# Optimization experiments

Measured on AMD Instinct MI355X. Metric: run time of the kernel, lower is better.

Reference implementation:

```python
import jax, jax.numpy as jnp
import numpy as np

D_MODEL = 1024
N_HEADS = 16
D_HEAD = D_MODEL // N_HEADS
EPS_LN = 1e-5
EPS_GATE = 1e-5
EPS_DEN = 1e-5


def setup_inputs() -> dict:
    key = jax.random.key(0)
    ks = jax.random.split(key, 4)
    B, T, D = 1, 2048, D_MODEL
    x = jax.random.normal(ks[0], (B, T, D), dtype=jnp.float32)
    # Linear weights scaled like torch default init (~1/sqrt(fan_in))
    s = 1.0 / np.sqrt(D)
    qkv_w = jax.random.normal(ks[1], (3 * D, D), dtype=jnp.float32) * s
    gate_w = jax.random.normal(ks[2], (D, D), dtype=jnp.float32) * s
    proj_w = jax.random.normal(ks[3], (D, D), dtype=jnp.float32) * s
    return {
        "x": x,
        "ln_g": jnp.ones((D,), jnp.float32),
        "ln_b": jnp.zeros((D,), jnp.float32),
        "qkv_w": qkv_w,
        "qkv_b": jnp.zeros((3 * D,), jnp.float32),
        "gate_w": gate_w,
        "gate_b": jnp.zeros((D,), jnp.float32),
        "proj_w": proj_w,
        "proj_b": jnp.zeros((D,), jnp.float32),
    }


def _linear(x, w, b):
    # torch nn.Linear: y = x @ W^T + b, W is (out, in)
    return jnp.einsum("btd,od->bto", x, w) + b


def reference(x, ln_g, ln_b, qkv_w, qkv_b, gate_w, gate_b, proj_w, proj_b):
    B, T, D = x.shape
    H, Dh = N_HEADS, D_HEAD

    # LayerNorm
    mu = jnp.mean(x, axis=-1, keepdims=True)
    var = jnp.mean((x - mu) ** 2, axis=-1, keepdims=True)
    x_norm = (x - mu) / jnp.sqrt(var + EPS_LN) * ln_g + ln_b

    qkv = _linear(x_norm, qkv_w, qkv_b)
    q, k, v = jnp.split(qkv, 3, axis=-1)

    # concept gate on raw x
    gate_sig = jax.nn.sigmoid(_linear(x, gate_w, gate_b))
    gate_norm = gate_sig / (jnp.mean(gate_sig, axis=-1, keepdims=True) + EPS_GATE)
    q = q * gate_norm
    k = k * gate_norm

    # (B,T,D) -> (B,H,T,Dh)
    def heads(t):
        return t.reshape(B, T, H, Dh).transpose(0, 2, 1, 3)

    q, k, v = heads(q).astype(jnp.float32), heads(k).astype(jnp.float32), heads(v).astype(jnp.float32)

    q = jax.nn.elu(q) + 1.0
    k = jax.nn.elu(k) + 1.0

    # causal linear attention via cumsum of outer products (same math as source)
    kv = jnp.einsum("bhtd,bhtm->bhtdm", k, v)        # (B,H,T,Dh,Dh)
    kv_cum = jnp.cumsum(kv, axis=2)
    out_num = jnp.einsum("bhtd,bhtdm->bhtm", q, kv_cum)
    k_cum = jnp.cumsum(k, axis=2)
    out_den = jnp.einsum("bhtd,bhtd->bht", q, k_cum)[..., None] + EPS_DEN
    out = out_num / out_den                           # (B,H,T,Dh)

    out = out.astype(x_norm.dtype).transpose(0, 2, 1, 3).reshape(B, T, D)
    return _linear(out, proj_w, proj_b)
```

## Files before the change

kernel.cpp:

```cpp
#include <hip/hip_runtime.h>
#include <hip/hip_bf16.h>
#include <math.h>

#define T_SEQ 2048
#define DM 1024
#define NH 16
#define DH 64
#define CHUNK 64
#define NCHUNK (T_SEQ / CHUNK)

typedef __hip_bfloat16 bf16;
typedef __attribute__((ext_vector_type(8))) short short8;
typedef __attribute__((ext_vector_type(4))) short short4v;
typedef __attribute__((ext_vector_type(4))) float f32x4;

static __device__ __forceinline__ short f2b_bits(float f) {
  bf16 t = __float2bfloat16(f);
  short s;
  __builtin_memcpy(&s, &t, 2);
  return s;
}
static __device__ __forceinline__ float b2f(short s) {
  unsigned int u = ((unsigned int)(unsigned short)s) << 16;
  float f;
  __builtin_memcpy(&f, &u, 4);
  return f;
}

static __device__ __forceinline__ float gelu1(float raw, float gate, float inv) {
  float x = raw * gate * inv;
  return x > 0.f ? x + 1.f : __expf(x);
}

static __device__ __forceinline__ void gload16(const void* g, void* l) {
  __builtin_amdgcn_global_load_lds((const __attribute__((address_space(1))) void*)g,
                                   (__attribute__((address_space(3))) void*)l, 16, 0, 0);
}

#define PREP_WBLOCKS (5 * DM * DM / 4 / 256)
__global__ __launch_bounds__(256) void prep_kernel(
    const float* __restrict__ x, const float* __restrict__ g,
    const float* __restrict__ b, const float* __restrict__ qkv_w,
    const float* __restrict__ gate_w, const float* __restrict__ proj_w,
    bf16* __restrict__ xn, bf16* __restrict__ xbf,
    bf16* __restrict__ wqkv, bf16* __restrict__ wgate, bf16* __restrict__ wproj,
    float* __restrict__ gate_accum) {
  const int blk = blockIdx.x;
  if (blk < T_SEQ) {
    const int row = blk;
    if (row < 8) gate_accum[row * 256 + threadIdx.x] = 0.f;
    const float* xr = x + (size_t)row * DM;
    float vals[4];
    float s = 0.f, s2 = 0.f;
#pragma unroll
    for (int i = 0; i < 4; i++) {
      float v = xr[threadIdx.x + i * 256];
      vals[i] = v;
      s += v;
      s2 += v * v;
    }
#pragma unroll
    for (int m = 1; m < 64; m <<= 1) {
      s += __shfl_xor(s, m, 64);
      s2 += __shfl_xor(s2, m, 64);
    }
    __shared__ float red[8];
    const int wid = threadIdx.x >> 6;
    if ((threadIdx.x & 63) == 0) {
      red[wid] = s;
      red[4 + wid] = s2;
    }
    __syncthreads();
    s = red[0] + red[1] + red[2] + red[3];
    s2 = red[4] + red[5] + red[6] + red[7];
    const float mean = s * (1.f / DM);
    const float var = s2 * (1.f / DM) - mean * mean;
    const float rstd = rsqrtf(var + 1e-5f);
#pragma unroll
    for (int i = 0; i < 4; i++) {
      int idx = threadIdx.x + i * 256;
      float v = (vals[i] - mean) * rstd * g[idx] + b[idx];
      xn[(size_t)row * DM + idx] = __float2bfloat16(v);
      xbf[(size_t)row * DM + idx] = __float2bfloat16(vals[i]);
    }
  } else {
    constexpr int NQ = 3 * DM * DM / 4, NS = DM * DM / 4;
    int i = (blk - T_SEQ) * 256 + threadIdx.x;
    const float* src;
    bf16* dst;
    int j;
    if (i < NQ) { src = qkv_w; dst = wqkv; j = i; }
    else if (i < NQ + NS) { src = gate_w; dst = wgate; j = i - NQ; }
    else { src = proj_w; dst = wproj; j = i - NQ - NS; }
    float4 v = ((const float4*)src)[j];
    short4v sv;
    sv.x = f2b_bits(v.x); sv.y = f2b_bits(v.y); sv.z = f2b_bits(v.z); sv.w = f2b_bits(v.w);
    *(short4v*)&dst[j * 4] = sv;
  }
}

__global__ __launch_bounds__(256) void gemm_gateqkv(
    const bf16* __restrict__ xbf, const bf16* __restrict__ xn,
    const bf16* __restrict__ wg, const bf16* __restrict__ wq,
    const float* __restrict__ gate_b, const float* __restrict__ qkv_b,
    short* __restrict__ Gb, float* __restrict__ gate_accum,
    short* __restrict__ Qb, short* __restrict__ Kb, short* __restrict__ Vb) {
  constexpr int K = 1024;
  __shared__ __align__(16) short As[2 * 128 * 32];
  __shared__ __align__(16) short Bs[2 * 128 * 32];

  const int tid = threadIdx.x;
  const int wid = tid >> 6, lane = tid & 63;
  const int wm = wid >> 1, wn = wid & 1;
  const int lm = lane & 15, quad = lane >> 4;

  const bool isGate = blockIdx.y < 8;
  const int m0 = blockIdx.x * 128;
  const int n0 = isGate ? blockIdx.y * 128 : (blockIdx.y - 8) * 128;
  const short* Ag = (const short*)(isGate ? xbf : xn);
  const short* Wg = (const short*)(isGate ? wg : wq);

  f32x4 zero = {0.f, 0.f, 0.f, 0.f};
  f32x4 acc[4][4];
#pragma unroll
  for (int i = 0; i < 4; i++)
#pragma unroll
    for (int j = 0; j < 4; j++) acc[i][j] = zero;

  for (int kb = 0; kb < K; kb += 64) {
    __syncthreads();
#pragma unroll
    for (int sec = 0; sec < 2; sec++) {
#pragma unroll
      for (int it = 0; it < 2; it++) {
        const int idx = it * 256 + tid;
        const int row = idx >> 2, seg = (idx & 3) * 8;
        gload16(&Ag[(size_t)(m0 + row) * K + kb + sec * 32 + seg],
                &As[sec * 4096 + (it * 256 + wid * 64) * 8]);
        gload16(&Wg[(size_t)(n0 + row) * K + kb + sec * 32 + seg],
                &Bs[sec * 4096 + (it * 256 + wid * 64) * 8]);
      }
    }
    __syncthreads();
#pragma unroll
    for (int sec = 0; sec < 2; sec++) {
      short8 afr[4], bfr[4];
#pragma unroll
      for (int i = 0; i < 4; i++) {
        afr[i] = *(const short8*)&As[sec * 4096 + (wm * 64 + i * 16 + lm) * 32 + quad * 8];
        bfr[i] = *(const short8*)&Bs[sec * 4096 + (wn * 64 + i * 16 + lm) * 32 + quad * 8];
      }
#pragma unroll
      for (int i = 0; i < 4; i++)
#pragma unroll
        for (int j = 0; j < 4; j++)
          acc[i][j] = __builtin_amdgcn_mfma_f32_16x16x32_bf16(afr[i], bfr[j], acc[i][j], 0, 0, 0);
    }
  }

  if (isGate) {
    float* red = (float*)As;
    __syncthreads();
#pragma unroll
    for (int i = 0; i < 4; i++) {
#pragma unroll
      for (int r = 0; r < 4; r++) {
        const int rowl = wm * 64 + i * 16 + quad * 4 + r;
        const int row = m0 + rowl;
        float rp = 0.f;
#pragma unroll
        for (int j = 0; j < 4; j++) {
          const int col = n0 + wn * 64 + j * 16 + lm;
          float v = acc[i][j][r] + gate_b[col];
          float sig = 1.f / (1.f + __expf(-v));
          Gb[(size_t)row * DM + col] = f2b_bits(sig);
          rp += sig;
        }
        red[rowl * 32 + wn * 16 + lm] = rp;
      }
    }
    __syncthreads();
    if (tid < 128) {
      float s = 0.f;
#pragma unroll
      for (int t2 = 0; t2 < 32; t2++) s += red[tid * 32 + t2];
      atomicAdd(&gate_accum[m0 + tid], s);
    }
  } else {
#pragma unroll
    for (int i = 0; i < 4; i++) {
      const int rbase = m0 + wm * 64 + i * 16 + quad * 4;
#pragma unroll
      for (int j = 0; j < 4; j++) {
        const int col = n0 + wn * 64 + j * 16 + lm;
        const float bval = qkv_b[col];
#pragma unroll
        for (int r = 0; r < 4; r++) {
          const int row = rbase + r;
          const short bv = f2b_bits(acc[i][j][r] + bval);
          if (col < DM) {
            const int d = col;
            Qb[((size_t)(d >> 6) * T_SEQ + row) * DH + (d & 63)] = bv;
          } else if (col < 2 * DM) {
            const int d = col - DM;
            Kb[((size_t)(d >> 6) * T_SEQ + row) * DH + (d & 63)] = bv;
          } else {
            const int d = col - 2 * DM;
            Vb[((size_t)(d >> 6) * T_SEQ + row) * DH + (d & 63)] = bv;
          }
        }
      }
    }
  }
}

__global__ __launch_bounds__(256) void gemm_proj(const bf16* __restrict__ A,
                                                 const bf16* __restrict__ W,
                                                 const float* __restrict__ bias,
                                                 float* __restrict__ Cout) {
  constexpr int K = 1024;
  __shared__ __align__(16) short As[2 * 64 * 32];
  __shared__ __align__(16) short Bs[2 * 128 * 32];

  const int tid = threadIdx.x;
  const int wid = tid >> 6, lane = tid & 63;
  const int wm = wid >> 1, wn = wid & 1;
  const int lm = lane & 15, quad = lane >> 4;

  const int m0 = blockIdx.x * 64;
  const int n0 = blockIdx.y * 128;
  const short* Ag = (const short*)A;
  const short* Wg = (const short*)W;

  f32x4 zero = {0.f, 0.f, 0.f, 0.f};
  f32x4 acc[2][4];
#pragma unroll
  for (int i = 0; i < 2; i++)
#pragma unroll
    for (int j = 0; j < 4; j++) acc[i][j] = zero;

  for (int kb = 0; kb < K; kb += 64) {
    __syncthreads();
#pragma unroll
    for (int sec = 0; sec < 2; sec++) {
      {
        const int row = tid >> 2, seg = (tid & 3) * 8;
        gload16(&Ag[(size_t)(m0 + row) * K + kb + sec * 32 + seg],
                &As[sec * 2048 + (wid * 64) * 8]);
      }
#pragma unroll
      for (int it = 0; it < 2; it++) {
        const int idx = it * 256 + tid;
        const int row = idx >> 2, seg = (idx & 3) * 8;
        gload16(&Wg[(size_t)(n0 + row) * K + kb + sec * 32 + seg],
                &Bs[sec * 4096 + (it * 256 + wid * 64) * 8]);
      }
    }
    __syncthreads();
#pragma unroll
    for (int sec = 0; sec < 2; sec++) {
      short8 afr[2], bfr[4];
#pragma unroll
      for (int i = 0; i < 2; i++)
        afr[i] = *(const short8*)&As[sec * 2048 + (wm * 32 + i * 16 + lm) * 32 + quad * 8];
#pragma unroll
      for (int j = 0; j < 4; j++)
        bfr[j] = *(const short8*)&Bs[sec * 4096 + (wn * 64 + j * 16 + lm) * 32 + quad * 8];
#pragma unroll
      for (int i = 0; i < 2; i++)
#pragma unroll
        for (int j = 0; j < 4; j++)
          acc[i][j] = __builtin_amdgcn_mfma_f32_16x16x32_bf16(afr[i], bfr[j], acc[i][j], 0, 0, 0);
    }
  }
#pragma unroll
  for (int i = 0; i < 2; i++) {
    const int rbase = m0 + wm * 32 + i * 16 + quad * 4;
#pragma unroll
    for (int j = 0; j < 4; j++) {
      const int col = n0 + wn * 64 + j * 16 + lm;
      const float bval = bias[col];
#pragma unroll
      for (int r = 0; r < 4; r++)
        Cout[(size_t)(rbase + r) * DM + col] = acc[i][j][r] + bval;
    }
  }
}

__global__ __launch_bounds__(256, 2) void chunk_sum_mm(const short* __restrict__ Kb,
                                                       const short* __restrict__ Gb,
                                                       const float* __restrict__ ga,
                                                       const short* __restrict__ Vb,
                                                       float* __restrict__ Skv,
                                                       float* __restrict__ Sk) {
  constexpr int STR = 68;
  __shared__ __align__(16) float Ks2[64 * STR];
  __shared__ __align__(16) float Vs2[64 * STR];
  const int b = blockIdx.x;
  const int h = b >> 5, c = b & 31;
  const int tid = threadIdx.x;
  const int ty = tid >> 4, tx = tid & 15;
  const int d0 = ty * 4, m0 = tx * 4;
  const int t0 = c * CHUNK;
  const size_t cb = ((size_t)h * T_SEQ + t0) * DH;
#pragma unroll
  for (int p = 0; p < 4; p++) {
    int f = p * 256 + tid, row = f >> 4, seg = (f & 15) * 4;
    const int t = t0 + row;
    short4v kr = *(const short4v*)&Kb[cb + row * 64 + seg];
    short4v gr = *(const short4v*)&Gb[(size_t)t * DM + h * 64 + seg];
    short4v vr = *(const short4v*)&Vb[cb + row * 64 + seg];
    const float inv = 1.f / (ga[t] * (1.f / DM) + 1e-5f);
    f32x4 kgv, vv;
#pragma unroll
    for (int e = 0; e < 4; e++) {
      kgv[e] = gelu1(b2f(kr[e]), b2f(gr[e]), inv);
      vv[e] = b2f(vr[e]);
    }
    *(f32x4*)&Ks2[row * STR + seg] = kgv;
    *(f32x4*)&Vs2[row * STR + seg] = vv;
  }
  __syncthreads();
  float acc[4][4] = {};
#pragma unroll 4
  for (int s = 0; s < 64; s++) {
    f32x4 kf = *(const f32x4*)&Ks2[s * STR + d0];
    f32x4 vf = *(const f32x4*)&Vs2[s * STR + m0];
#pragma unroll
    for (int i = 0; i < 4; i++)
#pragma unroll
      for (int j = 0; j < 4; j++) acc[i][j] += kf[i] * vf[j];
  }
  float* outp = Skv + (size_t)b * 4096;
#pragma unroll
  for (int i = 0; i < 4; i++) {
    f32x4 o = {acc[i][0], acc[i][1], acc[i][2], acc[i][3]};
    *(f32x4*)&outp[(d0 + i) * 64 + m0] = o;
  }
  if (tid < 64) {
    float ss = 0.f;
#pragma unroll 4
    for (int s = 0; s < 64; s++) ss += Ks2[s * STR + tid];
    Sk[b * 64 + tid] = ss;
  }
}

__global__ __launch_bounds__(256) void scan_excl(float* __restrict__ Skv,
                                                 float* __restrict__ Sk) {
  const int bid = blockIdx.x, tid = threadIdx.x;
  if (bid < 256) {
    const int id = bid * 256 + tid;
    const int h = id >> 12, e = id & 4095;
    float* base = Skv + (size_t)h * NCHUNK * 4096 + e;
    float v[NCHUNK];
#pragma unroll
    for (int c = 0; c < NCHUNK; c++) v[c] = base[(size_t)c * 4096];
    float run = 0.f;
#pragma unroll
    for (int c = 0; c < NCHUNK; c++) {
      float t = v[c];
      base[(size_t)c * 4096] = run;
      run += t;
    }
  } else {
    const int id = (bid - 256) * 256 + tid;
    const int h = id >> 6, e = id & 63;
    float* base = Sk + (size_t)h * NCHUNK * 64 + e;
    float v[NCHUNK];
#pragma unroll
    for (int c = 0; c < NCHUNK; c++) v[c] = base[c * 64];
    float run = 0.f;
#pragma unroll
    for (int c = 0; c < NCHUNK; c++) {
      float t = v[c];
      base[c * 64] = run;
      run += t;
    }
  }
}

__global__ __launch_bounds__(256, 2) void attn_mm(const short* __restrict__ Qb,
                                                  const short* __restrict__ Kb,
                                                  const short* __restrict__ Gb,
                                                  const float* __restrict__ ga,
                                                  const short* __restrict__ Vb,
                                                  const float* __restrict__ Skv,
                                                  const float* __restrict__ Sk,
                                                  bf16* __restrict__ O) {
  constexpr int STR = 68;
  __shared__ __align__(16) float Qs[64 * STR];
  __shared__ __align__(16) float Vs[64 * STR];
  __shared__ __align__(16) float KPs[64 * STR];
  __shared__ float denp[64 * 16];
  __shared__ float skp[64];
  __shared__ float den[64];
  const int b = blockIdx.x;
  const int h = b >> 5, c = b & 31;
  const int tid = threadIdx.x;
  const int ty = tid >> 4, tx = tid & 15;
  const int r0 = ty * 4, c0 = tx * 4, m0 = tx * 4;
  const int t0 = c * CHUNK;
  const size_t cb = ((size_t)h * T_SEQ + t0) * DH;
  const float* Pg = Skv + (size_t)b * 4096;

  short4v kreg[4], greg[4];
  float ireg[4];
#pragma unroll
  for (int p = 0; p < 4; p++) {
    int f = p * 256 + tid, row = f >> 4, seg = (f & 15) * 4;
    kreg[p] = *(const short4v*)&Kb[cb + row * 64 + seg];
    greg[p] = *(const short4v*)&Gb[(size_t)(t0 + row) * DM + h * 64 + seg];
    ireg[p] = 1.f / (ga[t0 + row] * (1.f / DM) + 1e-5f);
  }
#pragma unroll
  for (int p = 0; p < 4; p++) {
    int f = p * 256 + tid, row = f >> 4, seg = (f & 15) * 4;
    short4v qr = *(const short4v*)&Qb[cb + row * 64 + seg];
    short4v gq = *(const short4v*)&Gb[(size_t)(t0 + row) * DM + h * 64 + seg];
    short4v vr = *(const short4v*)&Vb[cb + row * 64 + seg];
    const float inv = 1.f / (ga[t0 + row] * (1.f / DM) + 1e-5f);
    f32x4 qgv, vv;
#pragma unroll
    for (int e = 0; e < 4; e++) {
      qgv[e] = gelu1(b2f(qr[e]), b2f(gq[e]), inv);
      vv[e] = b2f(vr[e]);
    }
    *(f32x4*)&Qs[row * STR + seg] = qgv;
    *(f32x4*)&Vs[row * STR + seg] = vv;
    *(f32x4*)&KPs[row * STR + seg] = *(const f32x4*)&Pg[row * 64 + seg];
  }
  if (tid < 64) skp[tid] = Sk[b * 64 + tid];
  __syncthreads();

  if (tid < 64) {
    float s = 1e-5f;
#pragma unroll 4
    for (int d = 0; d < 64; d++) s += Qs[tid * STR + d] * skp[d];
    den[tid] = s;
  }

  float accO[4][4] = {};
#pragma unroll 2
  for (int d0 = 0; d0 < 64; d0 += 4) {
    f32x4 qf[4], pf[4];
#pragma unroll
    for (int i = 0; i < 4; i++) qf[i] = *(const f32x4*)&Qs[(r0 + i) * STR + d0];
#pragma unroll
    for (int dd = 0; dd < 4; dd++) pf[dd] = *(const f32x4*)&KPs[(d0 + dd) * STR + m0];
#pragma unroll
    for (int i = 0; i < 4; i++)
#pragma unroll
      for (int j = 0; j < 4; j++)
        accO[i][j] += qf[i][0] * pf[0][j] + qf[i][1] * pf[1][j] +
                      qf[i][2] * pf[2][j] + qf[i][3] * pf[3][j];
  }
  __syncthreads();
#pragma unroll
  for (int p = 0; p < 4; p++) {
    int f = p * 256 + tid, row = f >> 4, seg = (f & 15) * 4;
    f32x4 kgv;
#pragma unroll
    for (int e = 0; e < 4; e++) kgv[e] = gelu1(b2f(kreg[p][e]), b2f(greg[p][e]), ireg[p]);
    *(f32x4*)&KPs[row * STR + seg] = kgv;
  }
  __syncthreads();

  float accS[4][4] = {};
#pragma unroll 2
  for (int d0 = 0; d0 < 64; d0 += 4) {
    f32x4 qf[4], kf[4];
#pragma unroll
    for (int i = 0; i < 4; i++) qf[i] = *(const f32x4*)&Qs[(r0 + i) * STR + d0];
#pragma unroll
    for (int j = 0; j < 4; j++) kf[j] = *(const f32x4*)&KPs[(c0 + j) * STR + d0];
#pragma unroll
    for (int i = 0; i < 4; i++)
#pragma unroll
      for (int j = 0; j < 4; j++)
        accS[i][j] += qf[i][0] * kf[j][0] + qf[i][1] * kf[j][1] +
                      qf[i][2] * kf[j][2] + qf[i][3] * kf[j][3];
  }
  float dp[4];
#pragma unroll
  for (int i = 0; i < 4; i++) {
    dp[i] = 0.f;
#pragma unroll
    for (int j = 0; j < 4; j++) {
      float v = (c0 + j) <= (r0 + i) ? accS[i][j] : 0.f;
      accS[i][j] = v;
      dp[i] += v;
    }
  }
  __syncthreads();
#pragma unroll
  for (int i = 0; i < 4; i++) {
    f32x4 sv = {accS[i][0], accS[i][1], accS[i][2], accS[i][3]};
    *(f32x4*)&Qs[(r0 + i) * STR + c0] = sv;
    denp[(r0 + i) * 16 + tx] = dp[i];
  }
  __syncthreads();
  if (tid < 64) {
    float s = den[tid];
#pragma unroll
    for (int t = 0; t < 16; t++) s += denp[tid * 16 + t];
    den[tid] = s;
  }

#pragma unroll 2
  for (int c4 = 0; c4 < 64; c4 += 4) {
    f32x4 sf[4], vf[4];
#pragma unroll
    for (int i = 0; i < 4; i++) sf[i] = *(const f32x4*)&Qs[(r0 + i) * STR + c4];
#pragma unroll
    for (int cc = 0; cc < 4; cc++) vf[cc] = *(const f32x4*)&Vs[(c4 + cc) * STR + m0];
#pragma unroll
    for (int i = 0; i < 4; i++)
#pragma unroll
      for (int j = 0; j < 4; j++)
        accO[i][j] += sf[i][0] * vf[0][j] + sf[i][1] * vf[1][j] +
                      sf[i][2] * vf[2][j] + sf[i][3] * vf[3][j];
  }
  __syncthreads();

#pragma unroll
  for (int i = 0; i < 4; i++) {
    const float inv = 1.f / den[r0 + i];
    short4v ov;
#pragma unroll
    for (int j = 0; j < 4; j++) ov[j] = f2b_bits(accO[i][j] * inv);
    *(short4v*)&O[(size_t)(t0 + r0 + i) * DM + h * 64 + m0] = ov;
  }
}

extern "C" void kernel_launch(void* const* d_in, const int* in_sizes, int n_in,
                              void* d_out, int out_size, void* d_ws, size_t ws_size,
                              hipStream_t stream) {
  (void)in_sizes; (void)n_in; (void)out_size; (void)ws_size;
  const float* x      = (const float*)d_in[0];
  const float* ln_g   = (const float*)d_in[1];
  const float* ln_b   = (const float*)d_in[2];
  const float* qkv_w  = (const float*)d_in[3];
  const float* qkv_b  = (const float*)d_in[4];
  const float* gate_w = (const float*)d_in[5];
  const float* gate_b = (const float*)d_in[6];
  const float* proj_w = (const float*)d_in[7];
  const float* proj_b = (const float*)d_in[8];
  float* out = (float*)d_out;

  char* ws = (char*)d_ws;
  size_t off = 0;
  auto alloc = [&](size_t bytes) {
    void* p = ws + off;
    off += (bytes + 255) & ~(size_t)255;
    return p;
  };
  bf16*  xn       = (bf16*)alloc((size_t)T_SEQ * DM * 2);
  bf16*  xbf      = (bf16*)alloc((size_t)T_SEQ * DM * 2);
  bf16*  wqkv     = (bf16*)alloc((size_t)3 * DM * DM * 2);
  bf16*  wgate    = (bf16*)alloc((size_t)DM * DM * 2);
  bf16*  wproj    = (bf16*)alloc((size_t)DM * DM * 2);
  short* Gb       = (short*)alloc((size_t)T_SEQ * DM * 2);
  float* gate_accum = (float*)alloc((size_t)T_SEQ * 4);
  short* Qb       = (short*)alloc((size_t)T_SEQ * DM * 2);
  short* Kb       = (short*)alloc((size_t)T_SEQ * DM * 2);
  short* Vb       = (short*)alloc((size_t)T_SEQ * DM * 2);
  bf16*  Obuf     = (bf16*)alloc((size_t)T_SEQ * DM * 2);
  float* Skv      = (float*)alloc((size_t)NH * NCHUNK * 4096 * 4);
  float* Sk       = (float*)alloc((size_t)NH * NCHUNK * 64 * 4);

  prep_kernel<<<T_SEQ + PREP_WBLOCKS, 256, 0, stream>>>(
      x, ln_g, ln_b, qkv_w, gate_w, proj_w, xn, xbf, wqkv, wgate, wproj, gate_accum);
  gemm_gateqkv<<<dim3(16, 32), 256, 0, stream>>>(xbf, xn, wgate, wqkv, gate_b, qkv_b,
                                                 Gb, gate_accum, Qb, Kb, Vb);
  chunk_sum_mm<<<NH * NCHUNK, 256, 0, stream>>>(Kb, Gb, gate_accum, Vb, Skv, Sk);
  scan_excl<<<260, 256, 0, stream>>>(Skv, Sk);
  attn_mm<<<NH * NCHUNK, 256, 0, stream>>>(Qb, Kb, Gb, gate_accum, Vb, Skv, Sk, Obuf);
  gemm_proj<<<dim3(32, 8), 256, 0, stream>>>(Obuf, wproj, proj_b, out);
}
```

Measured before the change: 165.8 us.

## Fuse exclusive chunk-state scan into attention kernel and retile projection GEMM

Removes the separate scan_excl launch. Each attention block now sums the per-chunk KV and K states of all preceding chunks directly from global memory to build its own prefix. This saves one kernel launch and a read-write pass over Skv, but later chunks do redundant work that grows with chunk index, up to 31 loads of 16KB each. The projection GEMM also drops from 64x128 to 64x64 tiles with a 1D grid of 512 blocks, which should give better CU occupancy at the cost of more weight reloads.

```diff
diff --git a/kernel.cpp b/kernel.cpp
--- a/kernel.cpp
+++ b/kernel.cpp
@@ -26,12 +26,10 @@
   __builtin_memcpy(&f, &u, 4);
   return f;
 }
-
 static __device__ __forceinline__ float gelu1(float raw, float gate, float inv) {
   float x = raw * gate * inv;
   return x > 0.f ? x + 1.f : __expf(x);
 }
-
 static __device__ __forceinline__ void gload16(const void* g, void* l) {
   __builtin_amdgcn_global_load_lds((const __attribute__((address_space(1))) void*)g,
                                    (__attribute__((address_space(3))) void*)l, 16, 0, 0);
@@ -210,79 +208,6 @@
           }
         }
       }
-    }
-  }
-}
-
-__global__ __launch_bounds__(256) void gemm_proj(const bf16* __restrict__ A,
-                                                 const bf16* __restrict__ W,
-                                                 const float* __restrict__ bias,
-                                                 float* __restrict__ Cout) {
-  constexpr int K = 1024;
-  __shared__ __align__(16) short As[2 * 64 * 32];
-  __shared__ __align__(16) short Bs[2 * 128 * 32];
-
-  const int tid = threadIdx.x;
-  const int wid = tid >> 6, lane = tid & 63;
-  const int wm = wid >> 1, wn = wid & 1;
-  const int lm = lane & 15, quad = lane >> 4;
-
-  const int m0 = blockIdx.x * 64;
-  const int n0 = blockIdx.y * 128;
-  const short* Ag = (const short*)A;
-  const short* Wg = (const short*)W;
-
-  f32x4 zero = {0.f, 0.f, 0.f, 0.f};
-  f32x4 acc[2][4];
-#pragma unroll
-  for (int i = 0; i < 2; i++)
-#pragma unroll
-    for (int j = 0; j < 4; j++) acc[i][j] = zero;
-
-  for (int kb = 0; kb < K; kb += 64) {
-    __syncthreads();
-#pragma unroll
-    for (int sec = 0; sec < 2; sec++) {
-      {
-        const int row = tid >> 2, seg = (tid & 3) * 8;
-        gload16(&Ag[(size_t)(m0 + row) * K + kb + sec * 32 + seg],
-                &As[sec * 2048 + (wid * 64) * 8]);
-      }
-#pragma unroll
-      for (int it = 0; it < 2; it++) {
-        const int idx = it * 256 + tid;
-        const int row = idx >> 2, seg = (idx & 3) * 8;
-        gload16(&Wg[(size_t)(n0 + row) * K + kb + sec * 32 + seg],
-                &Bs[sec * 4096 + (it * 256 + wid * 64) * 8]);
-      }
-    }
-    __syncthreads();
-#pragma unroll
-    for (int sec = 0; sec < 2; sec++) {
-      short8 afr[2], bfr[4];
-#pragma unroll
-      for (int i = 0; i < 2; i++)
-        afr[i] = *(const short8*)&As[sec * 2048 + (wm * 32 + i * 16 + lm) * 32 + quad * 8];
-#pragma unroll
-      for (int j = 0; j < 4; j++)
-        bfr[j] = *(const short8*)&Bs[sec * 4096 + (wn * 64 + j * 16 + lm) * 32 + quad * 8];
-#pragma unroll
-      for (int i = 0; i < 2; i++)
-#pragma unroll
-        for (int j = 0; j < 4; j++)
-          acc[i][j] = __builtin_amdgcn_mfma_f32_16x16x32_bf16(afr[i], bfr[j], acc[i][j], 0, 0, 0);
-    }
-  }
-#pragma unroll
-  for (int i = 0; i < 2; i++) {
-    const int rbase = m0 + wm * 32 + i * 16 + quad * 4;
-#pragma unroll
-    for (int j = 0; j < 4; j++) {
-      const int col = n0 + wn * 64 + j * 16 + lm;
-      const float bval = bias[col];
-#pragma unroll
-      for (int r = 0; r < 4; r++)
-        Cout[(size_t)(rbase + r) * DM + col] = acc[i][j][r] + bval;
     }
   }
 }
@@ -342,40 +267,6 @@
 #pragma unroll 4
     for (int s = 0; s < 64; s++) ss += Ks2[s * STR + tid];
     Sk[b * 64 + tid] = ss;
-  }
-}
-
-__global__ __launch_bounds__(256) void scan_excl(float* __restrict__ Skv,
-                                                 float* __restrict__ Sk) {
-  const int bid = blockIdx.x, tid = threadIdx.x;
-  if (bid < 256) {
-    const int id = bid * 256 + tid;
-    const int h = id >> 12, e = id & 4095;
-    float* base = Skv + (size_t)h * NCHUNK * 4096 + e;
-    float v[NCHUNK];
-#pragma unroll
-    for (int c = 0; c < NCHUNK; c++) v[c] = base[(size_t)c * 4096];
-    float run = 0.f;
-#pragma unroll
-    for (int c = 0; c < NCHUNK; c++) {
-      float t = v[c];
-      base[(size_t)c * 4096] = run;
-      run += t;
-    }
-  } else {
-    const int id = (bid - 256) * 256 + tid;
-    const int h = id >> 6, e = id & 63;
-    float* base = Sk + (size_t)h * NCHUNK * 64 + e;
-    float v[NCHUNK];
-#pragma unroll
-    for (int c = 0; c < NCHUNK; c++) v[c] = base[c * 64];
-    float run = 0.f;
-#pragma unroll
-    for (int c = 0; c < NCHUNK; c++) {
-      float t = v[c];
-      base[c * 64] = run;
-      run += t;
-    }
   }
 }
 
@@ -401,20 +292,19 @@
   const int r0 = ty * 4, c0 = tx * 4, m0 = tx * 4;
   const int t0 = c * CHUNK;
   const size_t cb = ((size_t)h * T_SEQ + t0) * DH;
-  const float* Pg = Skv + (size_t)b * 4096;
 
   short4v kreg[4], greg[4];
   float ireg[4];
 #pragma unroll
-  for (int p = 0; p < 4; p++) {
-    int f = p * 256 + tid, row = f >> 4, seg = (f & 15) * 4;
-    kreg[p] = *(const short4v*)&Kb[cb + row * 64 + seg];
-    greg[p] = *(const short4v*)&Gb[(size_t)(t0 + row) * DM + h * 64 + seg];
-    ireg[p] = 1.f / (ga[t0 + row] * (1.f / DM) + 1e-5f);
-  }
-#pragma unroll
-  for (int p = 0; p < 4; p++) {
-    int f = p * 256 + tid, row = f >> 4, seg = (f & 15) * 4;
+  for (int q = 0; q < 4; q++) {
+    int f = q * 256 + tid, row = f >> 4, seg = (f & 15) * 4;
+    kreg[q] = *(const short4v*)&Kb[cb + row * 64 + seg];
+    greg[q] = *(const short4v*)&Gb[(size_t)(t0 + row) * DM + h * 64 + seg];
+    ireg[q] = 1.f / (ga[t0 + row] * (1.f / DM) + 1e-5f);
+  }
+#pragma unroll
+  for (int q = 0; q < 4; q++) {
+    int f = q * 256 + tid, row = f >> 4, seg = (f & 15) * 4;
     short4v qr = *(const short4v*)&Qb[cb + row * 64 + seg];
     short4v gq = *(const short4v*)&Gb[(size_t)(t0 + row) * DM + h * 64 + seg];
     short4v vr = *(const short4v*)&Vb[cb + row * 64 + seg];
@@ -427,9 +317,25 @@
     }
     *(f32x4*)&Qs[row * STR + seg] = qgv;
     *(f32x4*)&Vs[row * STR + seg] = vv;
-    *(f32x4*)&KPs[row * STR + seg] = *(const f32x4*)&Pg[row * 64 + seg];
-  }
-  if (tid < 64) skp[tid] = Sk[b * 64 + tid];
+  }
+  f32x4 preg[4];
+#pragma unroll
+  for (int g = 0; g < 4; g++) preg[g] = {0.f, 0.f, 0.f, 0.f};
+  for (int cc = 0; cc < c; cc++) {
+    const float* Pc = Skv + ((size_t)(h * NCHUNK + cc)) * 4096;
+#pragma unroll
+    for (int g = 0; g < 4; g++) preg[g] += *(const f32x4*)&Pc[g * 1024 + tid * 4];
+  }
+  if (tid < 64) {
+    float skpv = 0.f;
+    for (int cc = 0; cc < c; cc++) skpv += Sk[(h * NCHUNK + cc) * 64 + tid];
+    skp[tid] = skpv;
+  }
+#pragma unroll
+  for (int g = 0; g < 4; g++) {
+    const int E = g * 1024 + tid * 4;
+    *(f32x4*)&KPs[(E >> 6) * STR + (E & 63)] = preg[g];
+  }
   __syncthreads();
 
   if (tid < 64) {
@@ -456,11 +362,11 @@
   }
   __syncthreads();
 #pragma unroll
-  for (int p = 0; p < 4; p++) {
-    int f = p * 256 + tid, row = f >> 4, seg = (f & 15) * 4;
+  for (int q = 0; q < 4; q++) {
+    int f = q * 256 + tid, row = f >> 4, seg = (f & 15) * 4;
     f32x4 kgv;
 #pragma unroll
-    for (int e = 0; e < 4; e++) kgv[e] = gelu1(b2f(kreg[p][e]), b2f(greg[p][e]), ireg[p]);
+    for (int e = 0; e < 4; e++) kgv[e] = gelu1(b2f(kreg[q][e]), b2f(greg[q][e]), ireg[q]);
     *(f32x4*)&KPs[row * STR + seg] = kgv;
   }
   __syncthreads();
@@ -529,6 +435,72 @@
 #pragma unroll
     for (int j = 0; j < 4; j++) ov[j] = f2b_bits(accO[i][j] * inv);
     *(short4v*)&O[(size_t)(t0 + r0 + i) * DM + h * 64 + m0] = ov;
+  }
+}
+
+__global__ __launch_bounds__(256) void gemm_proj(const bf16* __restrict__ A,
+                                                 const bf16* __restrict__ W,
+                                                 const float* __restrict__ bias,
+                                                 float* __restrict__ Cout) {
+  constexpr int K = 1024;
+  __shared__ __align__(16) short As[2 * 64 * 32];
+  __shared__ __align__(16) short Bs[2 * 64 * 32];
+
+  const int tid = threadIdx.x;
+  const int wid = tid >> 6, lane = tid & 63;
+  const int wm = wid >> 1, wn = wid & 1;
+  const int lm = lane & 15, quad = lane >> 4;
+
+  const int m0 = (blockIdx.x & 31) * 64;
+  const int n0 = (blockIdx.x >> 5) * 64;
+  const short* Ag = (const short*)A;
+  const short* Wg = (const short*)W;
+
+  f32x4 zero = {0.f, 0.f, 0.f, 0.f};
+  f32x4 acc[2][2];
+#pragma unroll
+  for (int i = 0; i < 2; i++)
+#pragma unroll
+    for (int j = 0; j < 2; j++) acc[i][j] = zero;
+
+  for (int kb = 0; kb < K; kb += 64) {
+    __syncthreads();
+#pragma unroll
+    for (int sec = 0; sec < 2; sec++) {
+      const int row = tid >> 2, seg = (tid & 3) * 8;
+      gload16(&Ag[(size_t)(m0 + row) * K + kb + sec * 32 + seg],
+              &As[sec * 2048 + wid * 512]);
+      gload16(&Wg[(size_t)(n0 + row) * K + kb + sec * 32 + seg],
+              &Bs[sec * 2048 + wid * 512]);
+    }
+    __syncthreads();
+#pragma unroll
+    for (int sec = 0; sec < 2; sec++) {
+      short8 afr[2], bfr[2];
+#pragma unroll
+      for (int i = 0; i < 2; i++)
+        afr[i] = *(const short8*)&As[sec * 2048 + (wm * 32 + i * 16 + lm) * 32 + quad * 8];
+#pragma unroll
+      for (int j = 0; j < 2; j++)
+        bfr[j] = *(const short8*)&Bs[sec * 2048 + (wn * 32 + j * 16 + lm) * 32 + quad * 8];
+#pragma unroll
+      for (int i = 0; i < 2; i++)
+#pragma unroll
+        for (int j = 0; j < 2; j++)
+          acc[i][j] = __builtin_amdgcn_mfma_f32_16x16x32_bf16(afr[i], bfr[j], acc[i][j], 0, 0, 0);
+    }
+  }
+#pragma unroll
+  for (int i = 0; i < 2; i++) {
+    const int rbase = m0 + wm * 32 + i * 16 + quad * 4;
+#pragma unroll
+    for (int j = 0; j < 2; j++) {
+      const int col = n0 + wn * 32 + j * 16 + lm;
+      const float bval = bias[col];
+#pragma unroll
+      for (int r = 0; r < 4; r++)
+        Cout[(size_t)(rbase + r) * DM + col] = acc[i][j][r] + bval;
+    }
   }
 }
 
@@ -573,7 +545,6 @@
   gemm_gateqkv<<<dim3(16, 32), 256, 0, stream>>>(xbf, xn, wgate, wqkv, gate_b, qkv_b,
                                                  Gb, gate_accum, Qb, Kb, Vb);
   chunk_sum_mm<<<NH * NCHUNK, 256, 0, stream>>>(Kb, Gb, gate_accum, Vb, Skv, Sk);
-  scan_excl<<<260, 256, 0, stream>>>(Skv, Sk);
   attn_mm<<<NH * NCHUNK, 256, 0, stream>>>(Qb, Kb, Gb, gate_accum, Vb, Skv, Sk, Obuf);
-  gemm_proj<<<dim3(32, 8), 256, 0, stream>>>(Obuf, wproj, proj_b, out);
-}
+  gemm_proj<<<512, 256, 0, stream>>>(Obuf, wproj, proj_b, out);
+}
```

Measured after the change: 170.3 us. +2.7%, slower.
